# Performance work log

Hardware: AMD Instinct MI355X
Metric: run time of the kernel (lower is better)

## Reference

```python
import jax, jax.numpy as jnp
import numpy as np

NUM_EMBEDDINGS = 1024
EMBEDDING_DIM = 256
COMMITMENT_COST = 0.25


def setup_inputs() -> dict:
    key = jax.random.key(0)
    k1, k2 = jax.random.split(key)
    inputs = jax.random.normal(k1, (64, 32, 32, EMBEDDING_DIM), dtype=jnp.float32)
    embed = jax.random.normal(k2, (NUM_EMBEDDINGS, EMBEDDING_DIM), dtype=jnp.float32)
    return {"inputs": inputs, "embed": embed}


def reference(inputs, embed):
    # Eval-mode forward (no EMA buffer mutation), use_ema=True loss branch.
    input_shape = inputs.shape
    flat = inputs.reshape(-1, EMBEDDING_DIM)  # [N, d]
    distances = (
        jnp.sum(flat * flat, axis=1, keepdims=True)
        + jnp.sum(embed * embed, axis=1)
        - 2.0 * jnp.matmul(flat, embed.T)
    )
    encoding_indices = jnp.argmin(distances, axis=1)  # [N]
    # Gather codebook rows (equivalent to one-hot @ embed)
    quantized = embed[encoding_indices].reshape(input_shape)
    # use_ema branch: loss = commitment * mse(stop_grad(quantized), inputs)
    e_latent_loss = jnp.mean((jax.lax.stop_gradient(quantized) - inputs) ** 2)
    loss = COMMITMENT_COST * e_latent_loss
    # Straight-through estimator
    quantized_st = inputs + jax.lax.stop_gradient(quantized - inputs)
    # Perplexity from code usage histogram (== mean of one-hot encodings)
    n_tokens = flat.shape[0]
    counts = jax.ops.segment_sum(
        jnp.ones((n_tokens,), dtype=jnp.float32), encoding_indices,
        num_segments=NUM_EMBEDDINGS)
    avg_probs = counts / n_tokens
    perplexity = jnp.exp(-jnp.sum(avg_probs * jnp.log(avg_probs + 1e-10)))
    return quantized_st, loss, perplexity, encoding_indices
```

## Files before the change

### kernel.cpp

```cpp
#include <hip/hip_runtime.h>

#define NTOK 65536
#define DIM 256
#define KC 1024
#define EPS 0.08f

typedef __attribute__((ext_vector_type(8))) _Float16 f16x8;
typedef __attribute__((ext_vector_type(8))) unsigned short u16x8;
typedef __attribute__((ext_vector_type(4))) float f32x4;

static __device__ __forceinline__ unsigned short f16bits(float f) {
  _Float16 h = (_Float16)f;
  return __builtin_bit_cast(unsigned short, h);
}
static __device__ __forceinline__ unsigned packKey(float d, int code) {
  unsigned b = __float_as_uint(d);
  b = ((int)b < 0) ? ~b : (b | 0x80000000u);
  return (b & ~1023u) | (unsigned)code;
}
static __device__ __forceinline__ float decKey(unsigned k) {
  unsigned b = k & ~1023u;
  b = (b & 0x80000000u) ? (b ^ 0x80000000u) : ~b;
  return __uint_as_float(b);
}

__global__ __launch_bounds__(256) void vq_prep(
    const float* __restrict__ e, const float* __restrict__ x,
    unsigned short* __restrict__ eg, unsigned short* __restrict__ xg,
    float* __restrict__ esq, float* __restrict__ xsq,
    int* __restrict__ hist, int* __restrict__ fixCount) {
  if (blockIdx.x < 128) {
    const int gid = blockIdx.x * 256 + threadIdx.x;
    const int t = gid >> 5;
    const int o = gid & 31;
    const float4 v0 = *reinterpret_cast<const float4*>(&e[t * DIM + o * 8]);
    const float4 v1 = *reinterpret_cast<const float4*>(&e[t * DIM + o * 8 + 4]);
    u16x8 u;
    u[0] = f16bits(v0.x); u[1] = f16bits(v0.y); u[2] = f16bits(v0.z); u[3] = f16bits(v0.w);
    u[4] = f16bits(v1.x); u[5] = f16bits(v1.y); u[6] = f16bits(v1.z); u[7] = f16bits(v1.w);
    const int ctk = t >> 6, njj = (t >> 4) & 3, col = t & 15;
    const int s = o >> 2, kq = o & 3;
    char* dst = (char*)eg + ((ctk * 32 + s * 4 + njj) << 10) + ((kq * 16 + col) << 4);
    *reinterpret_cast<u16x8*>(dst) = u;
    float p = v0.x * v0.x + v0.y * v0.y + v0.z * v0.z + v0.w * v0.w +
              v1.x * v1.x + v1.y * v1.y + v1.z * v1.z + v1.w * v1.w;
#pragma unroll
    for (int m = 16; m > 0; m >>= 1) p += __shfl_xor(p, m, 64);
    if (o == 0) esq[t] = p;
    if (blockIdx.x < 4) hist[blockIdx.x * 256 + threadIdx.x] = 0;
    if (gid == 0) *fixCount = 0;
  } else {
    const int gid = (blockIdx.x - 128) * 256 + threadIdx.x;
    const int t = gid >> 5;
    const int o = gid & 31;
    const float4 v0 = *reinterpret_cast<const float4*>(&x[t * DIM + o * 8]);
    const float4 v1 = *reinterpret_cast<const float4*>(&x[t * DIM + o * 8 + 4]);
    u16x8 u;
    u[0] = f16bits(v0.x); u[1] = f16bits(v0.y); u[2] = f16bits(v0.z); u[3] = f16bits(v0.w);
    u[4] = f16bits(v1.x); u[5] = f16bits(v1.y); u[6] = f16bits(v1.z); u[7] = f16bits(v1.w);
    const int s = o >> 2, kq = o & 3;
    char* dst = (char*)xg + (((t >> 4) * 8 + s) << 10) + ((kq * 16 + (t & 15)) << 4);
    *reinterpret_cast<u16x8*>(dst) = u;
    float p = v0.x * v0.x + v0.y * v0.y + v0.z * v0.z + v0.w * v0.w +
              v1.x * v1.x + v1.y * v1.y + v1.z * v1.z + v1.w * v1.w;
#pragma unroll
    for (int m = 16; m > 0; m >>= 1) p += __shfl_xor(p, m, 64);
    if (o == 0) xsq[t] = p;
  }
}

__global__ __launch_bounds__(256, 4) void vq_argmin(
    const unsigned short* __restrict__ xg, const unsigned short* __restrict__ eg,
    const float* __restrict__ esq, unsigned int* __restrict__ rK1,
    unsigned int* __restrict__ rK2, unsigned int* __restrict__ rK3) {
  const int lane = threadIdx.x & 63, w = threadIdx.x >> 6;
  const int col = lane & 15, kq = lane >> 4;
  const int g = blockIdx.x & 7;
  const int j = blockIdx.x >> 3;
  const int cp = j & 7;
  const int tb = g * 32 + (j >> 3);
  const int cbase = cp * 128 + w * 32;
  const int ctk = cbase >> 6;
  const int njb = (w & 1) * 2;
  const int pw = cp * 4 + w;

  f16x8 ae[8][2];
#pragma unroll
  for (int s = 0; s < 8; ++s)
#pragma unroll
    for (int cg = 0; cg < 2; ++cg) {
      const char* ap =
          (const char*)eg + ((ctk * 32 + s * 4 + njb + cg) << 10) + (lane << 4);
      asm volatile("global_load_dwordx4 %0, %1, off"
                   : "=v"(ae[s][cg]) : "v"(ap) : "memory");
    }
  float esr[2][4];
#pragma unroll
  for (int cg = 0; cg < 2; ++cg)
#pragma unroll
    for (int r = 0; r < 4; ++r)
      esr[cg][r] = esq[cbase + cg * 16 + kq * 4 + r];
  asm volatile("s_waitcnt vmcnt(0)" ::: "memory");
  __builtin_amdgcn_sched_barrier(0);

#pragma unroll 2
  for (int i = 0; i < 16; ++i) {
    const int tsub = tb * 16 + i;
    f32x4 acc[2];
    acc[0] = (f32x4){0.f, 0.f, 0.f, 0.f};
    acc[1] = (f32x4){0.f, 0.f, 0.f, 0.f};
#pragma unroll
    for (int s = 0; s < 8; ++s) {
      const f16x8 bx = *reinterpret_cast<const f16x8*>(
          (const char*)xg + ((tsub * 8 + s) << 10) + (lane << 4));
      acc[0] = __builtin_amdgcn_mfma_f32_16x16x32_f16(ae[s][0], bx, acc[0], 0, 0, 0);
      acc[1] = __builtin_amdgcn_mfma_f32_16x16x32_f16(ae[s][1], bx, acc[1], 0, 0, 0);
    }
    unsigned k1 = 0xFFFFFFFFu, k2 = 0xFFFFFFFFu, k3 = 0xFFFFFFFFu;
#pragma unroll
    for (int cg = 0; cg < 2; ++cg)
#pragma unroll
      for (int r = 0; r < 4; ++r) {
        const int code = cbase + cg * 16 + kq * 4 + r;
        const unsigned k = packKey(fmaf(-2.f, acc[cg][r], esr[cg][r]), code);
        if (k < k1) { k3 = k2; k2 = k1; k1 = k; }
        else if (k < k2) { k3 = k2; k2 = k; }
        else if (k < k3) { k3 = k; }
      }
#pragma unroll
    for (int m = 16; m <= 32; m <<= 1) {
      const unsigned o1 = __shfl_xor((int)k1, m, 64);
      const unsigned o2 = __shfl_xor((int)k2, m, 64);
      const unsigned o3 = __shfl_xor((int)k3, m, 64);
      const unsigned t1 = max(k1, o1), lo2 = min(k2, o2);
      const unsigned nm1 = min(k1, o1);
      const unsigned nm2 = min(t1, lo2);
      const unsigned nm3 = min(min(max(t1, lo2), max(k2, o2)), min(k3, o3));
      k1 = nm1; k2 = nm2; k3 = nm3;
    }
    if (kq == 0) {
      const int rb = pw * NTOK + tsub * 16 + col;
      rK1[rb] = k1; rK2[rb] = k2; rK3[rb] = k3;
    }
  }
}

__global__ __launch_bounds__(256) void vq_finish1(
    const unsigned int* __restrict__ rK1, const unsigned int* __restrict__ rK2,
    const unsigned int* __restrict__ rK3, const float* __restrict__ xsq,
    float* __restrict__ outIdxF, float* __restrict__ bestDist,
    int* __restrict__ hist, int* __restrict__ fixCount,
    unsigned int* __restrict__ fixList) {
  const int t = blockIdx.x * 256 + threadIdx.x;
  unsigned m1 = 0xFFFFFFFFu, m2 = 0xFFFFFFFFu, m3 = 0xFFFFFFFFu;
  unsigned minFlagK1 = 0xFFFFFFFFu;
#pragma unroll
  for (int p = 0; p < 32; ++p) {
    const int rb = p * NTOK + t;
    const unsigned a1 = rK1[rb], a2 = rK2[rb], a3 = rK3[rb];
    if (decKey(a3) - decKey(a1) < EPS) minFlagK1 = min(minFlagK1, a1);
    const unsigned t1 = max(m1, a1), lo2 = min(m2, a2);
    const unsigned nm1 = min(m1, a1);
    const unsigned nm2 = min(t1, lo2);
    const unsigned nm3 = min(min(max(t1, lo2), max(m2, a2)), min(m3, a3));
    m1 = nm1; m2 = nm2; m3 = nm3;
  }
  const int mi1 = (int)(m1 & 1023u);
  const float d1 = decKey(m1);
  outIdxF[t] = (float)mi1;
  bestDist[t] = xsq[t] + d1;
  atomicAdd(&hist[mi1], 1);
  if (decKey(m2) - d1 < EPS) {
    const bool full = (decKey(m3) - d1 < EPS) || (decKey(minFlagK1) - d1 < EPS);
    const int p = atomicAdd(fixCount, 1);
    fixList[p * 2] = (unsigned)t | (full ? 0x80000000u : 0u);
    fixList[p * 2 + 1] = m2 & 1023u;
  }
}

__global__ __launch_bounds__(256) void vq_fixup(
    const float* __restrict__ x, const float* __restrict__ e,
    const int* __restrict__ fixCount, const unsigned int* __restrict__ fixList,
    float* __restrict__ outIdxF, float* __restrict__ bestDist,
    int* __restrict__ hist) {
  const int n = *fixCount;
  const int tid = threadIdx.x;
  __shared__ float xrow[256];
  __shared__ float rv[4];
  __shared__ int ri[4];
  for (int it = blockIdx.x; it < n; it += gridDim.x) {
    const unsigned e0 = fixList[it * 2];
    const int t = (int)(e0 & 0x3FFFFFFFu);
    const bool full = (e0 >> 31) != 0u;
    if (!full) {
      if (tid < 64) {
        const int i1 = (int)outIdxF[t];
        const int i2 = (int)fixList[it * 2 + 1];
        const float4 xv = reinterpret_cast<const float4*>(&x[t * DIM])[tid];
        const float4 e1 = reinterpret_cast<const float4*>(&e[i1 * DIM])[tid];
        const float4 e2 = reinterpret_cast<const float4*>(&e[i2 * DIM])[tid];
        float d1 = (xv.x - e1.x) * (xv.x - e1.x) + (xv.y - e1.y) * (xv.y - e1.y) +
                   (xv.z - e1.z) * (xv.z - e1.z) + (xv.w - e1.w) * (xv.w - e1.w);
        float d2 = (xv.x - e2.x) * (xv.x - e2.x) + (xv.y - e2.y) * (xv.y - e2.y) +
                   (xv.z - e2.z) * (xv.z - e2.z) + (xv.w - e2.w) * (xv.w - e2.w);
#pragma unroll
        for (int m = 32; m > 0; m >>= 1) {
          d1 += __shfl_xor(d1, m, 64);
          d2 += __shfl_xor(d2, m, 64);
        }
        const bool swap2 = (d2 < d1) || (d2 == d1 && i2 < i1);
        if (tid == 0) {
          bestDist[t] = swap2 ? d2 : d1;
          if (swap2) {
            atomicSub(&hist[i1], 1);
            atomicAdd(&hist[i2], 1);
            outIdxF[t] = (float)i2;
          }
        }
      }
    } else {
      __syncthreads();
      if (tid < 64) ((float4*)xrow)[tid] = ((const float4*)&x[t * DIM])[tid];
      __syncthreads();
      float bv = 3.4e38f; int bi = 0;
      for (int c = tid; c < KC; c += 256) {
        float s = 0.f;
#pragma unroll
        for (int d = 0; d < DIM; d += 4) {
          const float4 ev = *(const float4*)&e[c * DIM + d];
          const float d0 = xrow[d] - ev.x, d1 = xrow[d + 1] - ev.y;
          const float d2 = xrow[d + 2] - ev.z, d3 = xrow[d + 3] - ev.w;
          s += d0 * d0 + d1 * d1 + d2 * d2 + d3 * d3;
        }
        if (s < bv) { bv = s; bi = c; }
      }
#pragma unroll
      for (int m = 1; m <= 32; m <<= 1) {
        const float ob = __shfl_xor(bv, m, 64);
        const int oi = __shfl_xor(bi, m, 64);
        if (ob < bv || (ob == bv && oi < bi)) { bv = ob; bi = oi; }
      }
      const int lane = tid & 63, wv = tid >> 6;
      if (lane == 0) { rv[wv] = bv; ri[wv] = bi; }
      __syncthreads();
      if (tid == 0) {
        float fb = rv[0]; int fi = ri[0];
        for (int k = 1; k < 4; ++k)
          if (rv[k] < fb || (rv[k] == fb && ri[k] < fi)) { fb = rv[k]; fi = ri[k]; }
        const int sOld = (int)outIdxF[t];
        bestDist[t] = fb;
        if (fi != sOld) {
          atomicSub(&hist[sOld], 1);
          atomicAdd(&hist[fi], 1);
          outIdxF[t] = (float)fi;
        }
      }
      __syncthreads();
    }
  }
}

__global__ __launch_bounds__(256) void vq_gather(
    const float* __restrict__ e, const float* __restrict__ outIdxF,
    float* __restrict__ outQ) {
  const int lane = threadIdx.x & 63, w = threadIdx.x >> 6;
  const int t0 = blockIdx.x * 64 + w * 16;
#pragma unroll
  for (int i = 0; i < 16; ++i) {
    const int t = t0 + i;
    const int id = (int)outIdxF[t];
    const float4 q = reinterpret_cast<const float4*>(&e[id * DIM])[lane];
    reinterpret_cast<float4*>(&outQ[t * DIM])[lane] = q;
  }
}

__global__ __launch_bounds__(1024) void vq_final(
    const int* __restrict__ hist, const float* __restrict__ bestDist,
    float* __restrict__ outLoss, float* __restrict__ outPerp) {
  const int tid = threadIdx.x;
  float ls = 0.f;
  for (int i = 0; i < 64; ++i) ls += bestDist[tid + i * 1024];
  const float p = (float)hist[tid] * (1.f / 65536.f);
  float ent = p * logf(p + 1e-10f);
#pragma unroll
  for (int o = 32; o > 0; o >>= 1) {
    ls += __shfl_down(ls, o, 64);
    ent += __shfl_down(ent, o, 64);
  }
  __shared__ float lbuf[16], ebuf[16];
  const int lane = tid & 63, wv = tid >> 6;
  if (lane == 0) { lbuf[wv] = ls; ebuf[wv] = ent; }
  __syncthreads();
  if (tid == 0) {
    float L = 0.f, E = 0.f;
    for (int i = 0; i < 16; ++i) { L += lbuf[i]; E += ebuf[i]; }
    *outLoss = 0.25f * (L / 16777216.f);
    *outPerp = expf(-E);
  }
}

extern "C" void kernel_launch(void* const* d_in, const int* in_sizes, int n_in,
                              void* d_out, int out_size, void* d_ws, size_t ws_size,
                              hipStream_t stream) {
  const float* x = (const float*)d_in[0];
  const float* e = (const float*)d_in[1];
  float* out = (float*)d_out;
  float* outQ = out;
  float* outLoss = out + 16777216;
  float* outPerp = out + 16777217;
  float* outIdxF = out + 16777218;

  unsigned short* xg = (unsigned short*)d_out;
  unsigned int* rK1 = (unsigned int*)(out + 8388608);
  unsigned int* rK2 = (unsigned int*)(out + 10485760);
  unsigned int* rK3 = (unsigned int*)(out + 12582912);

  char* ws = (char*)d_ws;
  int*   hist     = (int*)ws;
  float* esq      = (float*)(ws + 4096);
  float* xsq      = (float*)(ws + 8192);
  float* bestDist = (float*)(ws + 270336);
  int*   fixCount = (int*)(ws + 532480);
  unsigned int* fixList = (unsigned int*)(ws + 532496);
  unsigned short* e_f16 = (unsigned short*)(ws + 1056784);

  vq_prep<<<8320, 256, 0, stream>>>(e, x, e_f16, xg, esq, xsq, hist, fixCount);
  vq_argmin<<<2048, 256, 0, stream>>>(xg, e_f16, esq, rK1, rK2, rK3);
  vq_finish1<<<256, 256, 0, stream>>>(rK1, rK2, rK3, xsq, outIdxF, bestDist,
                                      hist, fixCount, fixList);
  vq_fixup<<<256, 256, 0, stream>>>(x, e, fixCount, fixList, outIdxF,
                                    bestDist, hist);
  vq_gather<<<1024, 256, 0, stream>>>(e, outIdxF, outQ);
  vq_final<<<1, 1024, 0, stream>>>(hist, bestDist, outLoss, outPerp);
}
```

Baseline: 172.7 us.

## Stage prep conversion through LDS, unify codebook layout, merge gather and final

The prep kernel now has each block convert 64 rows into the fp16 MFMA tile layout inside shared memory, then write contiguous 1KB tiles to global memory instead of scattered 16-byte stores. The codebook image uses the same tile layout as the inputs, and argmin's load addresses are updated to match. The top-3 insertion becomes branchless min/max, and the gather and final-reduction kernels merge into one launch to save a kernel boundary. The prep rows are now strided per thread, which may coalesce worse on the read side.

```diff
diff --git a/kernel.cpp b/kernel.cpp
--- a/kernel.cpp
+++ b/kernel.cpp
@@ -15,7 +15,7 @@
 }
 static __device__ __forceinline__ unsigned packKey(float d, int code) {
   unsigned b = __float_as_uint(d);
-  b = ((int)b < 0) ? ~b : (b | 0x80000000u);
+  b ^= (unsigned)((int)b >> 31) | 0x80000000u;
   return (b & ~1023u) | (unsigned)code;
 }
 static __device__ __forceinline__ float decKey(unsigned k) {
@@ -25,47 +25,54 @@
 }
 
 __global__ __launch_bounds__(256) void vq_prep(
-    const float* __restrict__ e, const float* __restrict__ x,
-    unsigned short* __restrict__ eg, unsigned short* __restrict__ xg,
-    float* __restrict__ esq, float* __restrict__ xsq,
+    const float* __restrict__ x, const float* __restrict__ e,
+    unsigned short* __restrict__ xg, unsigned short* __restrict__ eg,
+    float* __restrict__ xsq, float* __restrict__ esq,
     int* __restrict__ hist, int* __restrict__ fixCount) {
-  if (blockIdx.x < 128) {
-    const int gid = blockIdx.x * 256 + threadIdx.x;
-    const int t = gid >> 5;
-    const int o = gid & 31;
-    const float4 v0 = *reinterpret_cast<const float4*>(&e[t * DIM + o * 8]);
-    const float4 v1 = *reinterpret_cast<const float4*>(&e[t * DIM + o * 8 + 4]);
+  __shared__ char lds[32768];
+  const int tid = threadIdx.x;
+  const bool isE = blockIdx.x >= 1024;
+  const int rb = isE ? (int)blockIdx.x - 1024 : (int)blockIdx.x;
+  const float* src = isE ? e : x;
+  unsigned short* img = isE ? eg : xg;
+  float* sq = isE ? esq : xsq;
+
+  const int tk = tid >> 2;
+  const int part = tid & 3;
+  const int row = rb * 64 + tk;
+  const float4* srow =
+      reinterpret_cast<const float4*>(&src[row * DIM]) + part * 16;
+  float s = 0.f;
+#pragma unroll
+  for (int o = 0; o < 8; ++o) {
+    const float4 v0 = srow[o * 2];
+    const float4 v1 = srow[o * 2 + 1];
     u16x8 u;
-    u[0] = f16bits(v0.x); u[1] = f16bits(v0.y); u[2] = f16bits(v0.z); u[3] = f16bits(v0.w);
-    u[4] = f16bits(v1.x); u[5] = f16bits(v1.y); u[6] = f16bits(v1.z); u[7] = f16bits(v1.w);
-    const int ctk = t >> 6, njj = (t >> 4) & 3, col = t & 15;
-    const int s = o >> 2, kq = o & 3;
-    char* dst = (char*)eg + ((ctk * 32 + s * 4 + njj) << 10) + ((kq * 16 + col) << 4);
-    *reinterpret_cast<u16x8*>(dst) = u;
-    float p = v0.x * v0.x + v0.y * v0.y + v0.z * v0.z + v0.w * v0.w +
-              v1.x * v1.x + v1.y * v1.y + v1.z * v1.z + v1.w * v1.w;
-#pragma unroll
-    for (int m = 16; m > 0; m >>= 1) p += __shfl_xor(p, m, 64);
-    if (o == 0) esq[t] = p;
-    if (blockIdx.x < 4) hist[blockIdx.x * 256 + threadIdx.x] = 0;
-    if (gid == 0) *fixCount = 0;
-  } else {
-    const int gid = (blockIdx.x - 128) * 256 + threadIdx.x;
-    const int t = gid >> 5;
-    const int o = gid & 31;
-    const float4 v0 = *reinterpret_cast<const float4*>(&x[t * DIM + o * 8]);
-    const float4 v1 = *reinterpret_cast<const float4*>(&x[t * DIM + o * 8 + 4]);
-    u16x8 u;
-    u[0] = f16bits(v0.x); u[1] = f16bits(v0.y); u[2] = f16bits(v0.z); u[3] = f16bits(v0.w);
-    u[4] = f16bits(v1.x); u[5] = f16bits(v1.y); u[6] = f16bits(v1.z); u[7] = f16bits(v1.w);
-    const int s = o >> 2, kq = o & 3;
-    char* dst = (char*)xg + (((t >> 4) * 8 + s) << 10) + ((kq * 16 + (t & 15)) << 4);
-    *reinterpret_cast<u16x8*>(dst) = u;
-    float p = v0.x * v0.x + v0.y * v0.y + v0.z * v0.z + v0.w * v0.w +
-              v1.x * v1.x + v1.y * v1.y + v1.z * v1.z + v1.w * v1.w;
-#pragma unroll
-    for (int m = 16; m > 0; m >>= 1) p += __shfl_xor(p, m, 64);
-    if (o == 0) xsq[t] = p;
+    u[0] = f16bits(v0.x); u[1] = f16bits(v0.y);
+    u[2] = f16bits(v0.z); u[3] = f16bits(v0.w);
+    u[4] = f16bits(v1.x); u[5] = f16bits(v1.y);
+    u[6] = f16bits(v1.z); u[7] = f16bits(v1.w);
+    const int oo = part * 8 + o;
+    char* d = lds + ((tk >> 4) * 8 + (oo >> 2)) * 1024 +
+              (((oo & 3) * 16 + (tk & 15)) << 4);
+    *reinterpret_cast<u16x8*>(d) = u;
+    s += v0.x * v0.x + v0.y * v0.y + v0.z * v0.z + v0.w * v0.w +
+         v1.x * v1.x + v1.y * v1.y + v1.z * v1.z + v1.w * v1.w;
+  }
+  s += __shfl_xor(s, 1, 64);
+  s += __shfl_xor(s, 2, 64);
+  if (part == 0) sq[row] = s;
+  __syncthreads();
+  const int w = tid >> 6, lane = tid & 63;
+#pragma unroll
+  for (int r = 0; r < 8; ++r) {
+    const int c = r * 4 + w;
+    *reinterpret_cast<u16x8*>((char*)img + (rb * 32 + c) * 1024 + lane * 16) =
+        *reinterpret_cast<const u16x8*>(lds + c * 1024 + lane * 16);
+  }
+  if (isE) {
+    if (blockIdx.x < 1028) hist[(blockIdx.x - 1024) * 256 + tid] = 0;
+    if (blockIdx.x == 1024 && tid == 0) *fixCount = 0;
   }
 }
 
@@ -80,8 +87,6 @@
   const int cp = j & 7;
   const int tb = g * 32 + (j >> 3);
   const int cbase = cp * 128 + w * 32;
-  const int ctk = cbase >> 6;
-  const int njb = (w & 1) * 2;
   const int pw = cp * 4 + w;
 
   f16x8 ae[8][2];
@@ -89,8 +94,8 @@
   for (int s = 0; s < 8; ++s)
 #pragma unroll
     for (int cg = 0; cg < 2; ++cg) {
-      const char* ap =
-          (const char*)eg + ((ctk * 32 + s * 4 + njb + cg) << 10) + (lane << 4);
+      const char* ap = (const char*)eg +
+                       (((cp * 8 + w * 2 + cg) * 8 + s) << 10) + (lane << 4);
       asm volatile("global_load_dwordx4 %0, %1, off"
                    : "=v"(ae[s][cg]) : "v"(ap) : "memory");
     }
@@ -123,9 +128,9 @@
       for (int r = 0; r < 4; ++r) {
         const int code = cbase + cg * 16 + kq * 4 + r;
         const unsigned k = packKey(fmaf(-2.f, acc[cg][r], esr[cg][r]), code);
-        if (k < k1) { k3 = k2; k2 = k1; k1 = k; }
-        else if (k < k2) { k3 = k2; k2 = k; }
-        else if (k < k3) { k3 = k; }
+        const unsigned mx1 = max(k1, k); k1 = min(k1, k);
+        const unsigned mx2 = max(k2, mx1); k2 = min(k2, mx1);
+        k3 = min(k3, mx2);
       }
 #pragma unroll
     for (int m = 16; m <= 32; m <<= 1) {
@@ -139,8 +144,8 @@
       k1 = nm1; k2 = nm2; k3 = nm3;
     }
     if (kq == 0) {
-      const int rb = pw * NTOK + tsub * 16 + col;
-      rK1[rb] = k1; rK2[rb] = k2; rK3[rb] = k3;
+      const int rb2 = pw * NTOK + tsub * 16 + col;
+      rK1[rb2] = k1; rK2[rb2] = k2; rK3[rb2] = k3;
     }
   }
 }
@@ -260,42 +265,54 @@
   }
 }
 
-__global__ __launch_bounds__(256) void vq_gather(
+__global__ __launch_bounds__(256) void vq_tail(
     const float* __restrict__ e, const float* __restrict__ outIdxF,
-    float* __restrict__ outQ) {
-  const int lane = threadIdx.x & 63, w = threadIdx.x >> 6;
-  const int t0 = blockIdx.x * 64 + w * 16;
-#pragma unroll
-  for (int i = 0; i < 16; ++i) {
-    const int t = t0 + i;
-    const int id = (int)outIdxF[t];
-    const float4 q = reinterpret_cast<const float4*>(&e[id * DIM])[lane];
-    reinterpret_cast<float4*>(&outQ[t * DIM])[lane] = q;
-  }
-}
-
-__global__ __launch_bounds__(1024) void vq_final(
-    const int* __restrict__ hist, const float* __restrict__ bestDist,
-    float* __restrict__ outLoss, float* __restrict__ outPerp) {
+    const float* __restrict__ bestDist, const int* __restrict__ hist,
+    float* __restrict__ outQ, float* __restrict__ outLoss,
+    float* __restrict__ outPerp) {
   const int tid = threadIdx.x;
-  float ls = 0.f;
-  for (int i = 0; i < 64; ++i) ls += bestDist[tid + i * 1024];
-  const float p = (float)hist[tid] * (1.f / 65536.f);
-  float ent = p * logf(p + 1e-10f);
-#pragma unroll
-  for (int o = 32; o > 0; o >>= 1) {
-    ls += __shfl_down(ls, o, 64);
-    ent += __shfl_down(ent, o, 64);
-  }
-  __shared__ float lbuf[16], ebuf[16];
-  const int lane = tid & 63, wv = tid >> 6;
-  if (lane == 0) { lbuf[wv] = ls; ebuf[wv] = ent; }
-  __syncthreads();
-  if (tid == 0) {
-    float L = 0.f, E = 0.f;
-    for (int i = 0; i < 16; ++i) { L += lbuf[i]; E += ebuf[i]; }
-    *outLoss = 0.25f * (L / 16777216.f);
-    *outPerp = expf(-E);
+  if (blockIdx.x < 1024) {
+    const int lane = tid & 63, w = tid >> 6;
+    const int t0 = blockIdx.x * 64 + w * 16;
+#pragma unroll
+    for (int i = 0; i < 16; ++i) {
+      const int t = t0 + i;
+      const int id = (int)outIdxF[t];
+      const float4 q = reinterpret_cast<const float4*>(&e[id * DIM])[lane];
+      reinterpret_cast<float4*>(&outQ[t * DIM])[lane] = q;
+    }
+  } else {
+    float ls = 0.f;
+    const float4* bd4 = reinterpret_cast<const float4*>(bestDist);
+    for (int i = 0; i < 64; ++i) {
+      const float4 v = bd4[tid + i * 256];
+      ls += v.x + v.y + v.z + v.w;
+    }
+    const int4 h4 = reinterpret_cast<const int4*>(hist)[tid];
+    float ent = 0.f;
+    {
+      const float p0 = (float)h4.x * (1.f / 65536.f);
+      const float p1 = (float)h4.y * (1.f / 65536.f);
+      const float p2 = (float)h4.z * (1.f / 65536.f);
+      const float p3 = (float)h4.w * (1.f / 65536.f);
+      ent = p0 * logf(p0 + 1e-10f) + p1 * logf(p1 + 1e-10f) +
+            p2 * logf(p2 + 1e-10f) + p3 * logf(p3 + 1e-10f);
+    }
+#pragma unroll
+    for (int o = 32; o > 0; o >>= 1) {
+      ls += __shfl_down(ls, o, 64);
+      ent += __shfl_down(ent, o, 64);
+    }
+    __shared__ float lbuf[4], ebuf[4];
+    const int lane = tid & 63, wv = tid >> 6;
+    if (lane == 0) { lbuf[wv] = ls; ebuf[wv] = ent; }
+    __syncthreads();
+    if (tid == 0) {
+      float L = 0.f, E = 0.f;
+      for (int i = 0; i < 4; ++i) { L += lbuf[i]; E += ebuf[i]; }
+      *outLoss = 0.25f * (L / 16777216.f);
+      *outPerp = expf(-E);
+    }
   }
 }
 
@@ -324,12 +341,12 @@
   unsigned int* fixList = (unsigned int*)(ws + 532496);
   unsigned short* e_f16 = (unsigned short*)(ws + 1056784);
 
-  vq_prep<<<8320, 256, 0, stream>>>(e, x, e_f16, xg, esq, xsq, hist, fixCount);
+  vq_prep<<<1040, 256, 0, stream>>>(x, e, xg, e_f16, xsq, esq, hist, fixCount);
   vq_argmin<<<2048, 256, 0, stream>>>(xg, e_f16, esq, rK1, rK2, rK3);
   vq_finish1<<<256, 256, 0, stream>>>(rK1, rK2, rK3, xsq, outIdxF, bestDist,
                                       hist, fixCount, fixList);
   vq_fixup<<<256, 256, 0, stream>>>(x, e, fixCount, fixList, outIdxF,
                                     bestDist, hist);
-  vq_gather<<<1024, 256, 0, stream>>>(e, outIdxF, outQ);
-  vq_final<<<1, 1024, 0, stream>>>(hist, bestDist, outLoss, outPerp);
-}
+  vq_tail<<<1025, 256, 0, stream>>>(e, outIdxF, bestDist, hist, outQ,
+                                    outLoss, outPerp);
+}
```

After: 167.0 us. 3.3% less time.
